# Kernel tuning notes

Measured on AMD Instinct MI355X. Metric: run time of the kernel, lower is better.

Reference implementation:

```python
import jax, jax.numpy as jnp
import numpy as np

TOP_K = 8
N_EXPERTS = 64
ALPHA = 0.01

def setup_inputs() -> dict:
    key = jax.random.key(0)
    k1, k2 = jax.random.split(key)
    hidden_states = jax.random.normal(k1, (8, 4096, 1024), dtype=jnp.float32)
    weight = jax.random.normal(k2, (N_EXPERTS, 1024), dtype=jnp.float32) * 0.02
    return {"hidden_states": hidden_states, "weight": weight}

def reference(hidden_states, weight):
    bsz, seq_len, h = hidden_states.shape
    tokens = hidden_states.reshape(-1, h).astype(jnp.float32)          # [T, h]
    logits = tokens @ weight.astype(jnp.float32).T                     # [T, E]
    scores = jax.nn.softmax(logits, axis=-1)                           # [T, E]
    topk_weights, topk_indices = jax.lax.top_k(scores, TOP_K)          # [T, K]
    topk_indices = jnp.clip(topk_indices, 0, N_EXPERTS - 1)
    # renormalize top-k probabilities (norm_topk_prob=True, top_k>1)
    denom = topk_weights.sum(axis=-1, keepdims=True) + 1e-20
    topk_weights = topk_weights / denom
    # expert usage counts (bincount / scatter path)
    expert_counts = jnp.zeros((N_EXPERTS,), jnp.int32).at[topk_indices.reshape(-1)].add(1)
    # sequence aux loss (training path, seq_aux=True)
    idx_b = topk_indices.reshape(bsz, seq_len * TOP_K)                 # [B, S*K]
    ce = jnp.zeros((bsz, N_EXPERTS), jnp.float32)
    ce = ce.at[jnp.arange(bsz)[:, None], idx_b].add(1.0)
    ce = ce * (N_EXPERTS / (seq_len * TOP_K))
    scores_seq = scores.reshape(bsz, seq_len, N_EXPERTS)
    aux_loss = ((ce * scores_seq.mean(axis=1)).sum(axis=1)).mean() * ALPHA
    return (topk_indices.astype(jnp.int32),
            topk_weights.astype(hidden_states.dtype),
            aux_loss,
            expert_counts)
```

## Files before the change

### kernel.cpp

```cpp
#include <hip/hip_runtime.h>

#define NTOK 32768
#define HDIM 1024
#define NEXP 64
#define TK   8
#define NB   8
#define SEQ  4096

#define MB    128
#define KC    32
#define NCH   (HDIM / KC)
#define NTHR  512
#define NBLK  (NTOK / MB)

#define RING  5
#define CH_A  16384
#define CH_B  4096
#define CHSZ  (CH_A + 2 * CH_B)

typedef __attribute__((ext_vector_type(8))) short bf16x8;
typedef __attribute__((ext_vector_type(4))) float f32x4;

union BF8 { bf16x8 v; unsigned u[4]; };

__device__ inline unsigned f2bf(float x) {
    unsigned u = __float_as_uint(x);
    return (u + 0x7FFFu + ((u >> 16) & 1u)) >> 16;
}

__device__ inline void split4(float4 v, unsigned* hp, unsigned* lp) {
    unsigned h0 = f2bf(v.x), h1 = f2bf(v.y), h2 = f2bf(v.z), h3 = f2bf(v.w);
    unsigned l0 = f2bf(v.x - __uint_as_float(h0 << 16));
    unsigned l1 = f2bf(v.y - __uint_as_float(h1 << 16));
    unsigned l2 = f2bf(v.z - __uint_as_float(h2 << 16));
    unsigned l3 = f2bf(v.w - __uint_as_float(h3 << 16));
    hp[0] = h0 | (h1 << 16); hp[1] = h2 | (h3 << 16);
    lp[0] = l0 | (l1 << 16); lp[1] = l2 | (l3 << 16);
}

__device__ __forceinline__ void gl16(const void* g, void* l) {
    __builtin_amdgcn_global_load_lds(
        (const __attribute__((address_space(1))) void*)g,
        (__attribute__((address_space(3))) void*)l, 16, 0, 0);
}

__global__ void wsplit(const float* __restrict__ w,
                       unsigned short* __restrict__ whi,
                       unsigned short* __restrict__ wlo)
{
    int T = blockIdx.x * 256 + threadIdx.x;
    int slot = T >> 6, l = T & 63;
    int c = slot >> 3, s = (slot >> 2) & 1, n = slot & 3;
    int e = n * 16 + (l & 15);
    int k = c * 64 + s * 32 + (l >> 4) * 8;
    const float* src = w + (size_t)e * HDIM + k;
    float4 v0 = *(const float4*)(src);
    float4 v1 = *(const float4*)(src + 4);
    unsigned hp[4], lp[4];
    split4(v0, &hp[0], &lp[0]);
    split4(v1, &hp[2], &lp[2]);
    ((uint4*)whi)[T] = make_uint4(hp[0], hp[1], hp[2], hp[3]);
    ((uint4*)wlo)[T] = make_uint4(lp[0], lp[1], lp[2], lp[3]);
}

__global__ __launch_bounds__(NTHR, 2) void moe_gemm(
    const float* __restrict__ hidden,
    const unsigned short* __restrict__ w2hi,
    const unsigned short* __restrict__ w2lo,
    float* __restrict__ logits)
{
    __shared__ __align__(16) unsigned char smem[RING * CHSZ];

    const int tid   = threadIdx.x;
    const int w     = tid >> 6;
    const int l     = tid & 63;
    const int m     = l & 15;
    const int q     = l >> 4;
    const int wm    = w >> 1;
    const int wn    = w & 1;
    const int wbase = tid & 448;
    const size_t t0 = (size_t)blockIdx.x * MB;

    const unsigned short* bsrc = (w < 4) ? w2hi : w2lo;
    const int w4   = w & 3;
    const int bDst = CH_A + (w >> 2) * CH_B + w4 * 1024;

    auto stage = [&](int kk, unsigned char* nb) {
#pragma unroll
        for (int i = 0; i < 2; ++i) {
            int g  = i * NTHR + tid;
            int r  = g >> 3;
            int sp = (g & 7) ^ (r & 7);
            gl16(hidden + (t0 + r) * HDIM + kk * KC + sp * 4,
                 nb + (size_t)(i * NTHR + wbase) * 16);
        }
        gl16(bsrc + (size_t)kk * 2048 + (size_t)(w4 * 64 + l) * 8,
             nb + bDst);
    };

    f32x4 acc[2][2];
#pragma unroll
    for (int mt = 0; mt < 2; ++mt)
#pragma unroll
        for (int n = 0; n < 2; ++n) acc[mt][n] = (f32x4)0.f;

    stage(0, smem);
    stage(1, smem + CHSZ);
    stage(2, smem + 2 * CHSZ);

    int bufR = 0, bufW = 3;
    for (int kk = 0; kk < NCH; ++kk) {
        if (kk + 3 < NCH) {
            stage(kk + 3, smem + bufW * CHSZ);
            bufW = (bufW == RING - 1) ? 0 : bufW + 1;
        }
        if      (kk + 3 <  NCH) asm volatile("s_waitcnt vmcnt(9)" ::: "memory");
        else if (kk + 3 == NCH) asm volatile("s_waitcnt vmcnt(6)" ::: "memory");
        else if (kk + 2 == NCH) asm volatile("s_waitcnt vmcnt(3)" ::: "memory");
        else                    asm volatile("s_waitcnt vmcnt(0)" ::: "memory");
        __builtin_amdgcn_s_barrier();
        __builtin_amdgcn_sched_barrier(0);

        const unsigned char* Ab = smem + bufR * CHSZ;
        bufR = (bufR == RING - 1) ? 0 : bufR + 1;

        bf16x8 bh[2], bl[2];
#pragma unroll
        for (int n = 0; n < 2; ++n) {
            int off = CH_A + (wn * 2 + n) * 1024 + l * 16;
            bh[n] = *(const bf16x8*)(Ab + off);
            bl[n] = *(const bf16x8*)(Ab + CH_B + off);
        }

#pragma unroll
        for (int mt = 0; mt < 2; ++mt) {
            int r   = wm * 32 + mt * 16 + m;
            int sp0 = (q * 2)     ^ (r & 7);
            int sp1 = (q * 2 + 1) ^ (r & 7);
            float4 a0 = *(const float4*)(Ab + ((size_t)r * 8 + sp0) * 16);
            float4 a1 = *(const float4*)(Ab + ((size_t)r * 8 + sp1) * 16);
            BF8 ah, al;
            split4(a0, &ah.u[0], &al.u[0]);
            split4(a1, &ah.u[2], &al.u[2]);
#pragma unroll
            for (int n = 0; n < 2; ++n) {
                acc[mt][n] = __builtin_amdgcn_mfma_f32_16x16x32_bf16(ah.v, bh[n], acc[mt][n], 0, 0, 0);
                acc[mt][n] = __builtin_amdgcn_mfma_f32_16x16x32_bf16(al.v, bh[n], acc[mt][n], 0, 0, 0);
                acc[mt][n] = __builtin_amdgcn_mfma_f32_16x16x32_bf16(ah.v, bl[n], acc[mt][n], 0, 0, 0);
            }
        }
    }

#pragma unroll
    for (int mt = 0; mt < 2; ++mt)
#pragma unroll
        for (int n = 0; n < 2; ++n)
#pragma unroll
            for (int r = 0; r < 4; ++r)
                logits[(t0 + wm * 32 + mt * 16 + q * 4 + r) * NEXP
                       + wn * 32 + n * 16 + m] = acc[mt][n][r];
}

__global__ __launch_bounds__(512, 4) void moe_gate(
    const float* __restrict__ logits,
    float* __restrict__ out,
    float* __restrict__ ws)
{
    __shared__ float sLog[64 * 66];
    __shared__ float mxArr[64];
    __shared__ float smSum[NEXP];
    __shared__ int   hist[NEXP];

    const int tid = threadIdx.x;
    const int w   = tid >> 6;
    const int l   = tid & 63;
    const int t0  = blockIdx.x * 64;

    if (tid < NEXP) { smSum[tid] = 0.f; hist[tid] = 0; }

    const float4* src = (const float4*)(logits + (size_t)t0 * NEXP);
#pragma unroll
    for (int j = 0; j < 2; ++j) {
        int g = j * 512 + tid;
        float4 v = src[g];
        int r = g >> 4, c = (g & 15) * 4;
        float* d = &sLog[r * 66 + c];
        d[0] = v.x; d[1] = v.y; d[2] = v.z; d[3] = v.w;
    }
    __syncthreads();

    float mxKeep = 0.f;
    float regSm = 0.f;
    for (int j = 0; j < 8; ++j) {
        int t = w * 8 + j;
        float x = sLog[t * 66 + l];
        float mx = x;
#pragma unroll
        for (int off = 32; off; off >>= 1) mx = fmaxf(mx, __shfl_xor(mx, off));
        float p = __expf(x - mx);
        float sd = p;
#pragma unroll
        for (int off = 32; off; off >>= 1) sd += __shfl_xor(sd, off);
        regSm += p / sd;
        if (l == 0) mxArr[t] = mx;
        (void)mxKeep;
    }
    atomicAdd(&smSum[l], regSm);
    __syncthreads();

    if (w == 0) {
        const float mx = mxArr[l];
        unsigned long long s8[TK];
#pragma unroll
        for (int j = 0; j < TK; ++j) s8[j] = 0ull;
        for (int e = 0; e < NEXP; ++e) {
            float x = sLog[l * 66 + e];
            unsigned u = __float_as_uint(x);
            unsigned k32 = (u & 0x80000000u) ? ~u : (u | 0x80000000u);
            unsigned long long key = ((unsigned long long)k32 << 6)
                                   | (unsigned long long)(63 - e);
            if (key > s8[TK - 1]) {
#pragma unroll
                for (int j = 0; j < TK; ++j) {
                    unsigned long long hi = s8[j] > key ? s8[j] : key;
                    key = s8[j] > key ? key : s8[j];
                    s8[j] = hi;
                }
            }
        }
        float ev[TK]; int ei[TK]; float sum = 0.f;
#pragma unroll
        for (int j = 0; j < TK; ++j) {
            unsigned k32 = (unsigned)(s8[j] >> 6);
            unsigned u = (k32 >> 31) ? (k32 ^ 0x80000000u) : ~k32;
            ev[j] = __expf(__uint_as_float(u) - mx);
            sum += ev[j];
            ei[j] = 63 - (int)(s8[j] & 63ull);
        }
        int t = t0 + l;
        float4 i0 = make_float4((float)ei[0], (float)ei[1], (float)ei[2], (float)ei[3]);
        float4 i1 = make_float4((float)ei[4], (float)ei[5], (float)ei[6], (float)ei[7]);
        *(float4*)(out + (size_t)t * TK)     = i0;
        *(float4*)(out + (size_t)t * TK + 4) = i1;
        float rs = 1.f / (sum + 1e-20f);
        float4 w0 = make_float4(ev[0] * rs, ev[1] * rs, ev[2] * rs, ev[3] * rs);
        float4 w1 = make_float4(ev[4] * rs, ev[5] * rs, ev[6] * rs, ev[7] * rs);
        *(float4*)(out + (size_t)NTOK * TK + (size_t)t * TK)     = w0;
        *(float4*)(out + (size_t)NTOK * TK + (size_t)t * TK + 4) = w1;
#pragma unroll
        for (int j = 0; j < TK; ++j) atomicAdd(&hist[ei[j]], 1);
    }
    __syncthreads();

    if (tid < NEXP) {
        int b = blockIdx.x >> 6;
        atomicAdd(&ws[b * NEXP + tid], (float)hist[tid]);
        atomicAdd(&ws[NB * NEXP + b * NEXP + tid], smSum[tid]);
    }
}

__global__ void moe_finalize(const float* __restrict__ ws, float* __restrict__ out)
{
    int e = threadIdx.x;
    float cnt = 0.f, accv = 0.f;
#pragma unroll
    for (int b = 0; b < NB; ++b) {
        float c  = ws[b * NEXP + e];
        float sm = ws[NB * NEXP + b * NEXP + e];
        cnt += c;
        accv += c * sm;
    }
    out[(size_t)NTOK * TK * 2 + 1 + e] = cnt;
#pragma unroll
    for (int off = 32; off; off >>= 1) accv += __shfl_xor(accv, off);
    if (e == 0) {
        float aux = 0.01f * accv * ((float)NEXP / ((float)SEQ * (float)TK))
                    / (float)SEQ / (float)NB;
        out[(size_t)NTOK * TK * 2] = aux;
    }
}

extern "C" void kernel_launch(void* const* d_in, const int* in_sizes, int n_in,
                              void* d_out, int out_size, void* d_ws, size_t ws_size,
                              hipStream_t stream)
{
    const float* hidden = (const float*)d_in[0];
    const float* weight = (const float*)d_in[1];
    float* out  = (float*)d_out;
    float* wsf  = (float*)d_ws;
    unsigned short* w2hi = (unsigned short*)(wsf + 2 * NB * NEXP);
    unsigned short* w2lo = w2hi + NEXP * HDIM;
    float* logits = (float*)(w2lo + NEXP * HDIM);

    hipMemsetAsync(d_ws, 0, 2 * NB * NEXP * sizeof(float), stream);
    wsplit<<<32, 256, 0, stream>>>(weight, w2hi, w2lo);
    moe_gemm<<<NBLK, NTHR, 0, stream>>>(hidden, w2hi, w2lo, logits);
    moe_gate<<<NTOK / 64, 512, 0, stream>>>(logits, out, wsf);
    moe_finalize<<<1, 64, 0, stream>>>(wsf, out);
}
```

Measured before the change: 235.0 us.

## Replace LDS ring-buffer staging with direct register double-buffered global loads

The GEMM kernel drops its 5-stage LDS ring filled by global_load_lds, along with the vmcnt waits and barriers. Each wave now loads its own A rows and the pre-split B fragments straight from global memory into registers, double-buffered across K chunks. Launch bounds rise to 4 blocks per CU because no shared memory is used. This removes LDS traffic and block-wide syncs, but loses cross-wave sharing of the A and B tiles and relies on cache for reuse, with uncoalesced-ish 32B row segments per lane.

```diff
diff --git a/kernel.cpp b/kernel.cpp
--- a/kernel.cpp
+++ b/kernel.cpp
@@ -12,11 +12,6 @@
 #define NCH   (HDIM / KC)
 #define NTHR  512
 #define NBLK  (NTOK / MB)
-
-#define RING  5
-#define CH_A  16384
-#define CH_B  4096
-#define CHSZ  (CH_A + 2 * CH_B)
 
 typedef __attribute__((ext_vector_type(8))) short bf16x8;
 typedef __attribute__((ext_vector_type(4))) float f32x4;
@@ -36,12 +31,6 @@
     unsigned l3 = f2bf(v.w - __uint_as_float(h3 << 16));
     hp[0] = h0 | (h1 << 16); hp[1] = h2 | (h3 << 16);
     lp[0] = l0 | (l1 << 16); lp[1] = l2 | (l3 << 16);
-}
-
-__device__ __forceinline__ void gl16(const void* g, void* l) {
-    __builtin_amdgcn_global_load_lds(
-        (const __attribute__((address_space(1))) void*)g,
-        (__attribute__((address_space(3))) void*)l, 16, 0, 0);
 }
 
 __global__ void wsplit(const float* __restrict__ w,
@@ -63,39 +52,30 @@
     ((uint4*)wlo)[T] = make_uint4(lp[0], lp[1], lp[2], lp[3]);
 }
 
-__global__ __launch_bounds__(NTHR, 2) void moe_gemm(
+__global__ __launch_bounds__(NTHR, 4) void moe_gemm(
     const float* __restrict__ hidden,
     const unsigned short* __restrict__ w2hi,
     const unsigned short* __restrict__ w2lo,
     float* __restrict__ logits)
 {
-    __shared__ __align__(16) unsigned char smem[RING * CHSZ];
-
-    const int tid   = threadIdx.x;
-    const int w     = tid >> 6;
-    const int l     = tid & 63;
-    const int m     = l & 15;
-    const int q     = l >> 4;
-    const int wm    = w >> 1;
-    const int wn    = w & 1;
-    const int wbase = tid & 448;
+    const int tid = threadIdx.x;
+    const int w   = tid >> 6;
+    const int l   = tid & 63;
+    const int m   = l & 15;
+    const int q   = l >> 4;
+    const int wm  = w >> 1;
+    const int wn  = w & 1;
     const size_t t0 = (size_t)blockIdx.x * MB;
 
-    const unsigned short* bsrc = (w < 4) ? w2hi : w2lo;
-    const int w4   = w & 3;
-    const int bDst = CH_A + (w >> 2) * CH_B + w4 * 1024;
-
-    auto stage = [&](int kk, unsigned char* nb) {
-#pragma unroll
-        for (int i = 0; i < 2; ++i) {
-            int g  = i * NTHR + tid;
-            int r  = g >> 3;
-            int sp = (g & 7) ^ (r & 7);
-            gl16(hidden + (t0 + r) * HDIM + kk * KC + sp * 4,
-                 nb + (size_t)(i * NTHR + wbase) * 16);
-        }
-        gl16(bsrc + (size_t)kk * 2048 + (size_t)(w4 * 64 + l) * 8,
-             nb + bDst);
+    const float* aR0 = hidden + (t0 + wm * 32 + m) * HDIM + q * 8;
+    const float* aR1 = aR0 + 16 * HDIM;
+    const unsigned short* bBase = w2hi;
+    const unsigned short* lBase = w2lo;
+    const int bLane = (wn * 2) * 512 + l * 8;
+
+    struct Regs {
+        float4 a00, a01, a10, a11;
+        bf16x8 bh0, bh1, bl0, bl1;
     };
 
     f32x4 acc[2][2];
@@ -104,51 +84,46 @@
 #pragma unroll
         for (int n = 0; n < 2; ++n) acc[mt][n] = (f32x4)0.f;
 
-    stage(0, smem);
-    stage(1, smem + CHSZ);
-    stage(2, smem + 2 * CHSZ);
-
-    int bufR = 0, bufW = 3;
-    for (int kk = 0; kk < NCH; ++kk) {
-        if (kk + 3 < NCH) {
-            stage(kk + 3, smem + bufW * CHSZ);
-            bufW = (bufW == RING - 1) ? 0 : bufW + 1;
-        }
-        if      (kk + 3 <  NCH) asm volatile("s_waitcnt vmcnt(9)" ::: "memory");
-        else if (kk + 3 == NCH) asm volatile("s_waitcnt vmcnt(6)" ::: "memory");
-        else if (kk + 2 == NCH) asm volatile("s_waitcnt vmcnt(3)" ::: "memory");
-        else                    asm volatile("s_waitcnt vmcnt(0)" ::: "memory");
-        __builtin_amdgcn_s_barrier();
-        __builtin_amdgcn_sched_barrier(0);
-
-        const unsigned char* Ab = smem + bufR * CHSZ;
-        bufR = (bufR == RING - 1) ? 0 : bufR + 1;
-
-        bf16x8 bh[2], bl[2];
-#pragma unroll
-        for (int n = 0; n < 2; ++n) {
-            int off = CH_A + (wn * 2 + n) * 1024 + l * 16;
-            bh[n] = *(const bf16x8*)(Ab + off);
-            bl[n] = *(const bf16x8*)(Ab + CH_B + off);
-        }
-
-#pragma unroll
-        for (int mt = 0; mt < 2; ++mt) {
-            int r   = wm * 32 + mt * 16 + m;
-            int sp0 = (q * 2)     ^ (r & 7);
-            int sp1 = (q * 2 + 1) ^ (r & 7);
-            float4 a0 = *(const float4*)(Ab + ((size_t)r * 8 + sp0) * 16);
-            float4 a1 = *(const float4*)(Ab + ((size_t)r * 8 + sp1) * 16);
-            BF8 ah, al;
-            split4(a0, &ah.u[0], &al.u[0]);
-            split4(a1, &ah.u[2], &al.u[2]);
-#pragma unroll
-            for (int n = 0; n < 2; ++n) {
-                acc[mt][n] = __builtin_amdgcn_mfma_f32_16x16x32_bf16(ah.v, bh[n], acc[mt][n], 0, 0, 0);
-                acc[mt][n] = __builtin_amdgcn_mfma_f32_16x16x32_bf16(al.v, bh[n], acc[mt][n], 0, 0, 0);
-                acc[mt][n] = __builtin_amdgcn_mfma_f32_16x16x32_bf16(ah.v, bl[n], acc[mt][n], 0, 0, 0);
-            }
-        }
+    auto loadc = [&](int kk, Regs& R) {
+        R.a00 = *(const float4*)(aR0 + kk * KC);
+        R.a01 = *(const float4*)(aR0 + kk * KC + 4);
+        R.a10 = *(const float4*)(aR1 + kk * KC);
+        R.a11 = *(const float4*)(aR1 + kk * KC + 4);
+        int s = kk * 4 * 512 + bLane;
+        R.bh0 = *(const bf16x8*)(bBase + s);
+        R.bh1 = *(const bf16x8*)(bBase + s + 512);
+        R.bl0 = *(const bf16x8*)(lBase + s);
+        R.bl1 = *(const bf16x8*)(lBase + s + 512);
+    };
+
+    auto comp = [&](const Regs& R) {
+        BF8 ah, al;
+        split4(R.a00, &ah.u[0], &al.u[0]);
+        split4(R.a01, &ah.u[2], &al.u[2]);
+        acc[0][0] = __builtin_amdgcn_mfma_f32_16x16x32_bf16(ah.v, R.bh0, acc[0][0], 0, 0, 0);
+        acc[0][0] = __builtin_amdgcn_mfma_f32_16x16x32_bf16(al.v, R.bh0, acc[0][0], 0, 0, 0);
+        acc[0][0] = __builtin_amdgcn_mfma_f32_16x16x32_bf16(ah.v, R.bl0, acc[0][0], 0, 0, 0);
+        acc[0][1] = __builtin_amdgcn_mfma_f32_16x16x32_bf16(ah.v, R.bh1, acc[0][1], 0, 0, 0);
+        acc[0][1] = __builtin_amdgcn_mfma_f32_16x16x32_bf16(al.v, R.bh1, acc[0][1], 0, 0, 0);
+        acc[0][1] = __builtin_amdgcn_mfma_f32_16x16x32_bf16(ah.v, R.bl1, acc[0][1], 0, 0, 0);
+        split4(R.a10, &ah.u[0], &al.u[0]);
+        split4(R.a11, &ah.u[2], &al.u[2]);
+        acc[1][0] = __builtin_amdgcn_mfma_f32_16x16x32_bf16(ah.v, R.bh0, acc[1][0], 0, 0, 0);
+        acc[1][0] = __builtin_amdgcn_mfma_f32_16x16x32_bf16(al.v, R.bh0, acc[1][0], 0, 0, 0);
+        acc[1][0] = __builtin_amdgcn_mfma_f32_16x16x32_bf16(ah.v, R.bl0, acc[1][0], 0, 0, 0);
+        acc[1][1] = __builtin_amdgcn_mfma_f32_16x16x32_bf16(ah.v, R.bh1, acc[1][1], 0, 0, 0);
+        acc[1][1] = __builtin_amdgcn_mfma_f32_16x16x32_bf16(al.v, R.bh1, acc[1][1], 0, 0, 0);
+        acc[1][1] = __builtin_amdgcn_mfma_f32_16x16x32_bf16(ah.v, R.bl1, acc[1][1], 0, 0, 0);
+    };
+
+    Regs RA, RB;
+    loadc(0, RA);
+#pragma unroll 2
+    for (int kk = 0; kk < NCH; kk += 2) {
+        loadc(kk + 1, RB);
+        comp(RA);
+        if (kk + 2 < NCH) loadc(kk + 2, RA);
+        comp(RB);
     }
 
 #pragma unroll
@@ -189,7 +164,6 @@
     }
     __syncthreads();
 
-    float mxKeep = 0.f;
     float regSm = 0.f;
     for (int j = 0; j < 8; ++j) {
         int t = w * 8 + j;
@@ -203,7 +177,6 @@
         for (int off = 32; off; off >>= 1) sd += __shfl_xor(sd, off);
         regSm += p / sd;
         if (l == 0) mxArr[t] = mx;
-        (void)mxKeep;
     }
     atomicAdd(&smSum[l], regSm);
     __syncthreads();
```

Result: slower. 248.9 us (+5.9%).
